# Performance work log

Hardware: AMD Instinct MI355X
Metric: run time of the kernel (lower is better)

The kernel has to match this reference:

```python
import jax, jax.numpy as jnp
import numpy as np

N_NODES = 100000
N_EDGES = 3200000
IN_DIM = 64
HID = 64


def setup_inputs() -> dict:
    key = jax.random.key(0)
    ks = jax.random.split(key, 12)
    x = jax.random.normal(ks[0], (N_NODES, IN_DIM), dtype=jnp.float32)
    edge_index = jax.random.randint(ks[1], (2, N_EDGES), 0, N_NODES, dtype=jnp.int64)
    tau = jax.random.uniform(ks[2], (N_NODES, 1), dtype=jnp.float32)
    d1 = IN_DIM + 1  # augmented feature dim
    s1 = 1.0 / np.sqrt(d1)
    s2 = 1.0 / np.sqrt(HID)
    # SAGEConv: out = lin_l(mean_aggr) + lin_r(x); bias lives in lin_l. Weights stored [in, out].
    W1l = jax.random.uniform(ks[3], (d1, HID), jnp.float32, -s1, s1)
    b1l = jax.random.uniform(ks[4], (HID,), jnp.float32, -s1, s1)
    W1r = jax.random.uniform(ks[5], (d1, HID), jnp.float32, -s1, s1)
    W2l = jax.random.uniform(ks[6], (HID, HID), jnp.float32, -s2, s2)
    b2l = jax.random.uniform(ks[7], (HID,), jnp.float32, -s2, s2)
    W2r = jax.random.uniform(ks[8], (HID, HID), jnp.float32, -s2, s2)
    Wfc = jax.random.uniform(ks[9], (HID, 1), jnp.float32, -s2, s2)
    bfc = jax.random.uniform(ks[10], (1,), jnp.float32, -s2, s2)
    return {"x": x, "edge_index": edge_index, "tau": tau,
            "W1l": W1l, "b1l": b1l, "W1r": W1r,
            "W2l": W2l, "b2l": b2l, "W2r": W2r,
            "Wfc": Wfc, "bfc": bfc}


def _sage_conv(x, src, dst, Wl, bl, Wr, n_nodes):
    # mean aggregation of source-node features onto target nodes
    summed = jax.ops.segment_sum(x[src], dst, num_segments=n_nodes)  # [N, d]
    deg = jax.ops.segment_sum(jnp.ones(src.shape[0], x.dtype), dst, num_segments=n_nodes)
    mean = summed / jnp.maximum(deg, 1.0)[:, None]
    return mean @ Wl + bl + x @ Wr


def reference(x, edge_index, tau, W1l, b1l, W1r, W2l, b2l, W2r, Wfc, bfc):
    src, dst = edge_index[0], edge_index[1]
    n = x.shape[0]
    h = jnp.concatenate([x, tau], axis=1)  # augment_features: append tau column
    h = jax.nn.relu(_sage_conv(h, src, dst, W1l, b1l, W1r, n))
    h = jax.nn.relu(_sage_conv(h, src, dst, W2l, b2l, W2r, n))
    return h @ Wfc + bfc  # [N, 1]
```

## Files before the change

### kernel.cpp

```cpp
#include <hip/hip_runtime.h>
#include <hip/hip_bf16.h>
#include <hip/hip_fp16.h>
#include <hip/hip_fp8.h>


#define BSH 7
#define NBKT 782
#define NBLK 512
#define PER 6250
#define CAP 6144
#define AB2 256

typedef _Float16 half8 __attribute__((ext_vector_type(8)));
typedef float floatx4 __attribute__((ext_vector_type(4)));
typedef float floatx2 __attribute__((ext_vector_type(2)));

struct h4s { __half2 lo, hi; };

#if __has_builtin(__builtin_amdgcn_cvt_pk_f32_fp8)
template <bool HI>
__device__ __forceinline__ float2 f8x2_to_f2(int v) {
    floatx2 r = __builtin_amdgcn_cvt_pk_f32_fp8(v, HI);
    return make_float2(r.x, r.y);
}
#else
template <bool HI>
__device__ __forceinline__ float2 f8x2_to_f2(int v) {
    unsigned short u = HI ? (unsigned short)(((unsigned)v) >> 16)
                          : (unsigned short)(v & 0xFFFF);
    __half2_raw r = __hip_cvt_fp8x2_to_halfraw2((__hip_fp8x2_storage_t)u, __HIP_E4M3);
    return __half22float2(*(__half2*)&r);
}
#endif

#if __has_builtin(__builtin_amdgcn_cvt_pk_fp8_f32)
__device__ __forceinline__ unsigned f4_to_f8x4(float a, float b, float c, float d) {
    int lo = __builtin_amdgcn_cvt_pk_fp8_f32(a, b, 0, false);
    return (unsigned)__builtin_amdgcn_cvt_pk_fp8_f32(c, d, lo, true);
}
__device__ __forceinline__ unsigned char f_to_f8(float a) {
    return (unsigned char)(__builtin_amdgcn_cvt_pk_fp8_f32(a, a, 0, false) & 0xFF);
}
#else
__device__ __forceinline__ unsigned f4_to_f8x4(float a, float b, float c, float d) {
    unsigned lo = (unsigned)__hip_cvt_float2_to_fp8x2(make_float2(a, b), __HIP_SATFINITE, __HIP_E4M3);
    unsigned hi = (unsigned)__hip_cvt_float2_to_fp8x2(make_float2(c, d), __HIP_SATFINITE, __HIP_E4M3);
    return lo | (hi << 16);
}
__device__ __forceinline__ unsigned char f_to_f8(float a) {
    return (unsigned char)__hip_cvt_float_to_fp8(a, __HIP_SATFINITE, __HIP_E4M3);
}
#endif

__global__ __launch_bounds__(256) void k_histprep(
    const int* __restrict__ dst, int* __restrict__ histT, int E,
    const float* __restrict__ x, __half* __restrict__ xh,
    unsigned char* __restrict__ xf8, int n4,
    const float* __restrict__ W1l, const float* __restrict__ W1r,
    const float* __restrict__ W2l, const float* __restrict__ W2r,
    __half* __restrict__ wbuf1, __half* __restrict__ wbuf2) {
    if (blockIdx.x < NBLK) {
        __shared__ int h[NBKT];
        for (int i = threadIdx.x; i < NBKT; i += 256) h[i] = 0;
        __syncthreads();
        int lo = blockIdx.x * PER;
        int hi = lo + PER; if (hi > E) hi = E;
        for (int e = lo + threadIdx.x; e < hi; e += 256)
            atomicAdd(&h[dst[e] >> BSH], 1);
        __syncthreads();
        for (int k = threadIdx.x; k < NBKT; k += 256)
            histT[k * NBLK + blockIdx.x] = h[k];
    } else if (blockIdx.x < NBLK + 9) {
        int idx = (blockIdx.x - NBLK) * 256 + threadIdx.x;
        if (idx < 1280) {
            int lane = idx & 63;
            int nt = (idx >> 6) & 3;
            int kstep = idx >> 8;
            int col = nt * 16 + (lane & 15);
            int kbase = kstep * 32 + (lane >> 4) * 8;
#pragma unroll
            for (int j = 0; j < 8; ++j) {
                int k = kbase + j;
                float v;
                if (k < 64)        v = W1l[k * 64 + col];
                else if (k < 128)  v = W1r[(k - 64) * 64 + col];
                else if (k == 128) v = W1l[64 * 64 + col];
                else if (k == 129) v = W1r[64 * 64 + col];
                else v = 0.f;
                wbuf1[(size_t)idx * 8 + j] = __float2half(v);
            }
        } else if (idx < 1280 + 1024) {
            int i2 = idx - 1280;
            int lane = i2 & 63;
            int nt = (i2 >> 6) & 3;
            int kstep = i2 >> 8;
            int col = nt * 16 + (lane & 15);
            int kbase = kstep * 32 + (lane >> 4) * 8;
#pragma unroll
            for (int j = 0; j < 8; ++j) {
                int k = kbase + j;
                float v = (k < 64) ? W2l[k * 64 + col] : W2r[(k - 64) * 64 + col];
                wbuf2[(size_t)i2 * 8 + j] = __float2half(v);
            }
        }
    } else {
        int i = (blockIdx.x - NBLK - 9) * 256 + threadIdx.x;
        if (i < n4) {
            float4 v = ((const float4*)x)[i];
            ((__half2*)xh)[2 * i]     = __floats2half2_rn(v.x, v.y);
            ((__half2*)xh)[2 * i + 1] = __floats2half2_rn(v.z, v.w);
            ((unsigned*)xf8)[i] = f4_to_f8x4(v.x, v.y, v.z, v.w);
        }
    }
}


__global__ __launch_bounds__(NBLK) void k_scanblk(int* __restrict__ histT,
                                                  int* __restrict__ btot) {
    __shared__ int s[NBLK];
    int k = blockIdx.x, t = threadIdx.x;
    int v = histT[k * NBLK + t];
    s[t] = v;
    __syncthreads();
    for (int off = 1; off < NBLK; off <<= 1) {
        int u = (t >= off) ? s[t - off] : 0;
        __syncthreads();
        s[t] += u;
        __syncthreads();
    }
    histT[k * NBLK + t] = s[t] - v;
    if (t == NBLK - 1) btot[k] = s[t];
}

__global__ __launch_bounds__(1024) void k_scanbkt(const int* __restrict__ btot,
                                                  int* __restrict__ bstart) {
    __shared__ int s[1024];
    int t = threadIdx.x;
    int v = (t < NBKT) ? btot[t] : 0;
    s[t] = v;
    __syncthreads();
    for (int off = 1; off < 1024; off <<= 1) {
        int u = (t >= off) ? s[t - off] : 0;
        __syncthreads();
        s[t] += u;
        __syncthreads();
    }
    if (t < NBKT) bstart[t] = s[t] - v;
    if (t == NBKT - 1) bstart[NBKT] = s[t];
}

__global__ __launch_bounds__(256) void k_scatter(const int* __restrict__ src,
                                                 const int* __restrict__ dst,
                                                 const int* __restrict__ histT,
                                                 const int* __restrict__ bstart,
                                                 int* __restrict__ binned, int E) {
    __shared__ int sorted[PER];
    __shared__ int lstart[NBKT + 1];
    __shared__ int cur[NBKT];
    __shared__ int gst[NBKT];
    __shared__ int tsum[256];
    int b = blockIdx.x, t = threadIdx.x;
    int base = b * PER;
    int blen = E - base; if (blen > PER) blen = PER;

    for (int k = t; k < NBKT; k += 256) lstart[k] = 0;
    __syncthreads();
    for (int e = base + t; e < base + blen; e += 256)
        atomicAdd(&lstart[dst[e] >> BSH], 1);
    __syncthreads();
    int c0 = 0;
    int i0 = t * 4;
#pragma unroll
    for (int j = 0; j < 4; ++j)
        if (i0 + j < NBKT) c0 += lstart[i0 + j];
    tsum[t] = c0;
    __syncthreads();
    for (int off = 1; off < 256; off <<= 1) {
        int u = (t >= off) ? tsum[t - off] : 0;
        __syncthreads();
        tsum[t] += u;
        __syncthreads();
    }
    int running = tsum[t] - c0;
    __syncthreads();
#pragma unroll
    for (int j = 0; j < 4; ++j) {
        int i = i0 + j;
        if (i < NBKT) {
            int v = lstart[i];
            lstart[i] = running;
            running += v;
        }
    }
    __syncthreads();
    if (t == 0) lstart[NBKT] = blen;
    for (int k = t; k < NBKT; k += 256) {
        cur[k] = lstart[k];
        gst[k] = bstart[k] + histT[k * NBLK + b];
    }
    __syncthreads();
    for (int e = base + t; e < base + blen; e += 256) {
        int d = dst[e], s = src[e];
        int pos = atomicAdd(&cur[d >> BSH], 1);
        sorted[pos] = (s << BSH) | (d & ((1 << BSH) - 1));
    }
    __syncthreads();
    int qw = t >> 4, ql = t & 15;
    for (int k = qw; k < NBKT; k += 16) {
        int st = lstart[k];
        int ln = lstart[k + 1] - st;
        int gd = gst[k];
        for (int i = ql; i < ln; i += 16)
            binned[gd + i] = sorted[st + i];
    }
}

__global__ __launch_bounds__(512) void k_csr(int* __restrict__ binned,
                                             const int* __restrict__ bstart,
                                             int* __restrict__ nodeoff,
                                             int E, int N) {
    __shared__ int cnt[128], sarr[128], cur[128];
    __shared__ int sorted[CAP];
    int k = blockIdx.x, t = threadIdx.x;
    int lo = bstart[k], hi = bstart[k + 1];
    if (t < 128) cnt[t] = 0;
    __syncthreads();
    for (int eb = lo; eb < hi; eb += 512 * 4) {
        int e0 = eb + t, e1 = e0 + 512, e2 = e0 + 1024, e3 = e0 + 1536;
        int p0 = (e0 < hi) ? binned[e0] : -1;
        int p1 = (e1 < hi) ? binned[e1] : -1;
        int p2 = (e2 < hi) ? binned[e2] : -1;
        int p3 = (e3 < hi) ? binned[e3] : -1;
        if (p0 >= 0) atomicAdd(&cnt[p0 & 127], 1);
        if (p1 >= 0) atomicAdd(&cnt[p1 & 127], 1);
        if (p2 >= 0) atomicAdd(&cnt[p2 & 127], 1);
        if (p3 >= 0) atomicAdd(&cnt[p3 & 127], 1);
    }
    __syncthreads();
    if (t < 128) sarr[t] = cnt[t];
    __syncthreads();
    for (int off = 1; off < 128; off <<= 1) {
        int u = 0;
        if (t < 128 && t >= off) u = sarr[t - off];
        __syncthreads();
        if (t < 128) sarr[t] += u;
        __syncthreads();
    }
    if (t < 128) {
        int excl = sarr[t] - cnt[t];
        cur[t] = excl;
        int node = (k << BSH) + t;
        if (node < N) nodeoff[node] = lo + excl;
    }
    if (k == NBKT - 1 && t == 0) nodeoff[N] = E;
    __syncthreads();
    for (int eb = lo; eb < hi; eb += 512 * 4) {
        int e0 = eb + t, e1 = e0 + 512, e2 = e0 + 1024, e3 = e0 + 1536;
        int p0 = (e0 < hi) ? binned[e0] : -1;
        int p1 = (e1 < hi) ? binned[e1] : -1;
        int p2 = (e2 < hi) ? binned[e2] : -1;
        int p3 = (e3 < hi) ? binned[e3] : -1;
        if (p0 >= 0) { int pos = atomicAdd(&cur[p0 & 127], 1); if (pos < CAP) sorted[pos] = p0 >> BSH; }
        if (p1 >= 0) { int pos = atomicAdd(&cur[p1 & 127], 1); if (pos < CAP) sorted[pos] = p1 >> BSH; }
        if (p2 >= 0) { int pos = atomicAdd(&cur[p2 & 127], 1); if (pos < CAP) sorted[pos] = p2 >> BSH; }
        if (p3 >= 0) { int pos = atomicAdd(&cur[p3 & 127], 1); if (pos < CAP) sorted[pos] = p3 >> BSH; }
    }
    __syncthreads();
    int len = hi - lo; if (len > CAP) len = CAP;
    for (int i = t; i < len; i += 512)
        binned[lo + i] = sorted[i];
}


__global__ __launch_bounds__(AB2) void k_aggrb1(
    const int* __restrict__ nbr, const int* __restrict__ nodeoff,
    const unsigned char* __restrict__ xf8, const float* __restrict__ tau,
    __half* __restrict__ zm1, __half* __restrict__ mt1, int N) {
    int t = threadIdx.x;
    int lane = t & 63;
    int q = lane >> 4;
    int c = lane & 15;
    int g = c & 3;
    int ch = c >> 2;
    unsigned cb = (unsigned)(ch << 4);
    const char* xb = (const char*)xf8;
    int nb = blockIdx.x << 6;

    for (int p = (t >> 6); p < 16; p += (AB2 / 64)) {
        int ld = (p << 2) + q;
        int node = nb + ld;
        int off0 = 0, off1 = 0;
        if (node < N) { off0 = nodeoff[node]; off1 = nodeoff[node + 1]; }
        int d = off1 - off0;
        int dm = d;
        dm = max(dm, __shfl_xor(dm, 16, 64));
        dm = max(dm, __shfl_xor(dm, 32, 64));
        float4 A0 = {0.f, 0.f, 0.f, 0.f}, A1 = A0, A2 = A0, A3 = A0;
        float sumtau = 0.f;
        for (int base = 0; base < dm; base += 16) {
            int nmax = dm - base; if (nmax > 16) nmax = 16;
            int ng = (nmax + 3) >> 2;
            int s0 = base + g;
            int s1 = s0 + 4, s2 = s0 + 8, s3 = s0 + 12;
            bool v0 = s0 < d, v1 = s1 < d, v2 = s2 < d, v3 = s3 < d;
            int sx0, sx1, sx2, sx3;
            int4 r0, r1, r2, r3;
            sx0 = nbr[off0 + (v0 ? s0 : 0)];
            sx0 = v0 ? sx0 : 0;
            r0 = *(const int4*)(xb + (((unsigned)sx0 << 6) + cb));
            if (ng > 1) {
                sx1 = nbr[off0 + (v1 ? s1 : 0)];
                sx1 = v1 ? sx1 : 0;
                r1 = *(const int4*)(xb + (((unsigned)sx1 << 6) + cb));
            }
            if (ng > 2) {
                sx2 = nbr[off0 + (v2 ? s2 : 0)];
                sx2 = v2 ? sx2 : 0;
                r2 = *(const int4*)(xb + (((unsigned)sx2 << 6) + cb));
            }
            if (ng > 3) {
                sx3 = nbr[off0 + (v3 ? s3 : 0)];
                sx3 = v3 ? sx3 : 0;
                r3 = *(const int4*)(xb + (((unsigned)sx3 << 6) + cb));
            }
            if (ch == 0) {
                if (v0) sumtau += tau[sx0];
                if (ng > 1 && v1) sumtau += tau[sx1];
                if (ng > 2 && v2) sumtau += tau[sx2];
                if (ng > 3 && v3) sumtau += tau[sx3];
            }
            auto accum = [&](const int4& r) {
                float2 l0 = f8x2_to_f2<false>(r.x), h0 = f8x2_to_f2<true>(r.x);
                float2 l1 = f8x2_to_f2<false>(r.y), h1v = f8x2_to_f2<true>(r.y);
                float2 l2 = f8x2_to_f2<false>(r.z), h2v = f8x2_to_f2<true>(r.z);
                float2 l3 = f8x2_to_f2<false>(r.w), h3v = f8x2_to_f2<true>(r.w);
                A0.x += l0.x; A0.y += l0.y; A0.z += h0.x; A0.w += h0.y;
                A1.x += l1.x; A1.y += l1.y; A1.z += h1v.x; A1.w += h1v.y;
                A2.x += l2.x; A2.y += l2.y; A2.z += h2v.x; A2.w += h2v.y;
                A3.x += l3.x; A3.y += l3.y; A3.z += h3v.x; A3.w += h3v.y;
            };
            if (v0)            accum(r0);
            if (ng > 1 && v1)  accum(r1);
            if (ng > 2 && v2)  accum(r2);
            if (ng > 3 && v3)  accum(r3);
        }
#pragma unroll
        for (int off = 1; off <= 2; off <<= 1) {
            A0.x += __shfl_xor(A0.x, off, 64); A0.y += __shfl_xor(A0.y, off, 64);
            A0.z += __shfl_xor(A0.z, off, 64); A0.w += __shfl_xor(A0.w, off, 64);
            A1.x += __shfl_xor(A1.x, off, 64); A1.y += __shfl_xor(A1.y, off, 64);
            A1.z += __shfl_xor(A1.z, off, 64); A1.w += __shfl_xor(A1.w, off, 64);
            A2.x += __shfl_xor(A2.x, off, 64); A2.y += __shfl_xor(A2.y, off, 64);
            A2.z += __shfl_xor(A2.z, off, 64); A2.w += __shfl_xor(A2.w, off, 64);
            A3.x += __shfl_xor(A3.x, off, 64); A3.y += __shfl_xor(A3.y, off, 64);
            A3.z += __shfl_xor(A3.z, off, 64); A3.w += __shfl_xor(A3.w, off, 64);
            sumtau += __shfl_xor(sumtau, off, 64);
        }
        float inv = 1.f / fmaxf((float)d, 1.f);
        if (node < N) {
            float4 Aw = (g == 0) ? A0 : ((g == 1) ? A1 : ((g == 2) ? A2 : A3));
            h4s o;
            o.lo = __floats2half2_rn(Aw.x * inv, Aw.y * inv);
            o.hi = __floats2half2_rn(Aw.z * inv, Aw.w * inv);
            *(h4s*)(zm1 + (size_t)node * 64 + (ch << 4) + (g << 2)) = o;
            if (c == 0) mt1[node] = __float2half(sumtau * inv);
        }
    }
}

__global__ __launch_bounds__(AB2) void k_aggrb2(
    const int* __restrict__ nbr, const int* __restrict__ nodeoff,
    const unsigned char* __restrict__ h1f8, __half* __restrict__ zm2, int N) {
    int t = threadIdx.x;
    int lane = t & 63;
    int q = lane >> 4;
    int c = lane & 15;
    int g = c & 3;
    int ch = c >> 2;
    unsigned cb = (unsigned)(ch << 4);
    const char* hb = (const char*)h1f8;
    int nb = blockIdx.x << 6;

    for (int p = (t >> 6); p < 16; p += (AB2 / 64)) {
        int ld = (p << 2) + q;
        int node = nb + ld;
        int off0 = 0, off1 = 0;
        if (node < N) { off0 = nodeoff[node]; off1 = nodeoff[node + 1]; }
        int d = off1 - off0;
        int dm = d;
        dm = max(dm, __shfl_xor(dm, 16, 64));
        dm = max(dm, __shfl_xor(dm, 32, 64));
        float4 A0 = {0.f, 0.f, 0.f, 0.f}, A1 = A0, A2 = A0, A3 = A0;
        for (int base = 0; base < dm; base += 16) {
            int nmax = dm - base; if (nmax > 16) nmax = 16;
            int ng = (nmax + 3) >> 2;
            int s0 = base + g;
            int s1 = s0 + 4, s2 = s0 + 8, s3 = s0 + 12;
            bool v0 = s0 < d, v1 = s1 < d, v2 = s2 < d, v3 = s3 < d;
            int sx0, sx1, sx2, sx3;
            int4 r0, r1, r2, r3;
            sx0 = nbr[off0 + (v0 ? s0 : 0)];
            sx0 = v0 ? sx0 : 0;
            r0 = *(const int4*)(hb + (((unsigned)sx0 << 6) + cb));
            if (ng > 1) {
                sx1 = nbr[off0 + (v1 ? s1 : 0)];
                sx1 = v1 ? sx1 : 0;
                r1 = *(const int4*)(hb + (((unsigned)sx1 << 6) + cb));
            }
            if (ng > 2) {
                sx2 = nbr[off0 + (v2 ? s2 : 0)];
                sx2 = v2 ? sx2 : 0;
                r2 = *(const int4*)(hb + (((unsigned)sx2 << 6) + cb));
            }
            if (ng > 3) {
                sx3 = nbr[off0 + (v3 ? s3 : 0)];
                sx3 = v3 ? sx3 : 0;
                r3 = *(const int4*)(hb + (((unsigned)sx3 << 6) + cb));
            }
            auto accum = [&](const int4& r) {
                float2 l0 = f8x2_to_f2<false>(r.x), h0 = f8x2_to_f2<true>(r.x);
                float2 l1 = f8x2_to_f2<false>(r.y), h1v = f8x2_to_f2<true>(r.y);
                float2 l2 = f8x2_to_f2<false>(r.z), h2v = f8x2_to_f2<true>(r.z);
                float2 l3 = f8x2_to_f2<false>(r.w), h3v = f8x2_to_f2<true>(r.w);
                A0.x += l0.x; A0.y += l0.y; A0.z += h0.x; A0.w += h0.y;
                A1.x += l1.x; A1.y += l1.y; A1.z += h1v.x; A1.w += h1v.y;
                A2.x += l2.x; A2.y += l2.y; A2.z += h2v.x; A2.w += h2v.y;
                A3.x += l3.x; A3.y += l3.y; A3.z += h3v.x; A3.w += h3v.y;
            };
            if (v0)            accum(r0);
            if (ng > 1 && v1)  accum(r1);
            if (ng > 2 && v2)  accum(r2);
            if (ng > 3 && v3)  accum(r3);
        }
#pragma unroll
        for (int off = 1; off <= 2; off <<= 1) {
            A0.x += __shfl_xor(A0.x, off, 64); A0.y += __shfl_xor(A0.y, off, 64);
            A0.z += __shfl_xor(A0.z, off, 64); A0.w += __shfl_xor(A0.w, off, 64);
            A1.x += __shfl_xor(A1.x, off, 64); A1.y += __shfl_xor(A1.y, off, 64);
            A1.z += __shfl_xor(A1.z, off, 64); A1.w += __shfl_xor(A1.w, off, 64);
            A2.x += __shfl_xor(A2.x, off, 64); A2.y += __shfl_xor(A2.y, off, 64);
            A2.z += __shfl_xor(A2.z, off, 64); A2.w += __shfl_xor(A2.w, off, 64);
            A3.x += __shfl_xor(A3.x, off, 64); A3.y += __shfl_xor(A3.y, off, 64);
            A3.z += __shfl_xor(A3.z, off, 64); A3.w += __shfl_xor(A3.w, off, 64);
        }
        float inv = 1.f / fmaxf((float)d, 1.f);
        if (node < N) {
            float4 Aw = (g == 0) ? A0 : ((g == 1) ? A1 : ((g == 2) ? A2 : A3));
            h4s o;
            o.lo = __floats2half2_rn(Aw.x * inv, Aw.y * inv);
            o.hi = __floats2half2_rn(Aw.z * inv, Aw.w * inv);
            *(h4s*)(zm2 + (size_t)node * 64 + (ch << 4) + (g << 2)) = o;
        }
    }
}


__global__ __launch_bounds__(256) void k_gemm1(
    const __half* __restrict__ zm1, const __half* __restrict__ mt1,
    const __half* __restrict__ xh, const float* __restrict__ tau,
    const __half* __restrict__ wbuf1, const float* __restrict__ b1l,
    __half* __restrict__ h1, unsigned char* __restrict__ h1f8, int ntiles) {
    int tile = blockIdx.x * 4 + (threadIdx.x >> 6);
    if (tile >= ntiles) return;
    int lane = threadIdx.x & 63;
    int sub = lane & 15;
    int quad = lane >> 4;
    int row = tile * 16 + sub;

    floatx4 acc0 = {0.f, 0.f, 0.f, 0.f};
    floatx4 acc1 = {0.f, 0.f, 0.f, 0.f};
    floatx4 acc2 = {0.f, 0.f, 0.f, 0.f};
    floatx4 acc3 = {0.f, 0.f, 0.f, 0.f};

    const _Float16* zrow = (const _Float16*)zm1 + (size_t)row * 64 + quad * 8;
    const _Float16* xrow = (const _Float16*)xh + (size_t)row * 64 + quad * 8;
    const _Float16* wb = (const _Float16*)wbuf1 + (size_t)lane * 8;

    half8 amat[5];
    amat[0] = *(const half8*)(zrow);
    amat[1] = *(const half8*)(zrow + 32);
    amat[2] = *(const half8*)(xrow);
    amat[3] = *(const half8*)(xrow + 32);
    half8 a4 = {0, 0, 0, 0, 0, 0, 0, 0};
    if (quad == 0) {
        a4[0] = ((const _Float16*)mt1)[row];
        a4[1] = (_Float16)tau[row];
    }
    amat[4] = a4;

#pragma unroll
    for (int ks = 0; ks < 5; ++ks) {
        half8 a = amat[ks];
        half8 b0 = *(const half8*)(wb + (size_t)(ks * 4 + 0) * 512);
        half8 b1 = *(const half8*)(wb + (size_t)(ks * 4 + 1) * 512);
        half8 b2 = *(const half8*)(wb + (size_t)(ks * 4 + 2) * 512);
        half8 b3 = *(const half8*)(wb + (size_t)(ks * 4 + 3) * 512);
        acc0 = __builtin_amdgcn_mfma_f32_16x16x32_f16(a, b0, acc0, 0, 0, 0);
        acc1 = __builtin_amdgcn_mfma_f32_16x16x32_f16(a, b1, acc1, 0, 0, 0);
        acc2 = __builtin_amdgcn_mfma_f32_16x16x32_f16(a, b2, acc2, 0, 0, 0);
        acc3 = __builtin_amdgcn_mfma_f32_16x16x32_f16(a, b3, acc3, 0, 0, 0);
    }
    float bv0 = b1l[sub], bv1 = b1l[16 + sub], bv2 = b1l[32 + sub], bv3 = b1l[48 + sub];
#pragma unroll
    for (int reg = 0; reg < 4; ++reg) {
        int r = quad * 4 + reg;
        float v0 = fmaxf(acc0[reg] + bv0, 0.f);
        float v1 = fmaxf(acc1[reg] + bv1, 0.f);
        float v2 = fmaxf(acc2[reg] + bv2, 0.f);
        float v3 = fmaxf(acc3[reg] + bv3, 0.f);
        __half* orow = h1 + (size_t)(tile * 16 + r) * 64;
        orow[sub]      = __float2half(v0);
        orow[16 + sub] = __float2half(v1);
        orow[32 + sub] = __float2half(v2);
        orow[48 + sub] = __float2half(v3);
        unsigned char* orow8 = h1f8 + (size_t)(tile * 16 + r) * 64;
        orow8[sub]      = f_to_f8(v0);
        orow8[16 + sub] = f_to_f8(v1);
        orow8[32 + sub] = f_to_f8(v2);
        orow8[48 + sub] = f_to_f8(v3);
    }
}

__global__ __launch_bounds__(256) void k_gemm2(
    const __half* __restrict__ zm2, const __half* __restrict__ h1,
    const __half* __restrict__ wbuf2, const float* __restrict__ b2l,
    const float* __restrict__ Wfc, const float* __restrict__ bfc,
    float* __restrict__ out, int ntiles) {
    int tile = blockIdx.x * 4 + (threadIdx.x >> 6);
    if (tile >= ntiles) return;
    int lane = threadIdx.x & 63;
    int sub = lane & 15;
    int quad = lane >> 4;
    int row = tile * 16 + sub;

    floatx4 acc0 = {0.f, 0.f, 0.f, 0.f};
    floatx4 acc1 = {0.f, 0.f, 0.f, 0.f};
    floatx4 acc2 = {0.f, 0.f, 0.f, 0.f};
    floatx4 acc3 = {0.f, 0.f, 0.f, 0.f};

    const _Float16* zrow = (const _Float16*)zm2 + (size_t)row * 64 + quad * 8;
    const _Float16* hrow = (const _Float16*)h1 + (size_t)row * 64 + quad * 8;
    const _Float16* wb = (const _Float16*)wbuf2 + (size_t)lane * 8;

    half8 amat[4];
    amat[0] = *(const half8*)(zrow);
    amat[1] = *(const half8*)(zrow + 32);
    amat[2] = *(const half8*)(hrow);
    amat[3] = *(const half8*)(hrow + 32);

#pragma unroll
    for (int ks = 0; ks < 4; ++ks) {
        half8 a = amat[ks];
        half8 b0 = *(const half8*)(wb + (size_t)(ks * 4 + 0) * 512);
        half8 b1 = *(const half8*)(wb + (size_t)(ks * 4 + 1) * 512);
        half8 b2 = *(const half8*)(wb + (size_t)(ks * 4 + 2) * 512);
        half8 b3 = *(const half8*)(wb + (size_t)(ks * 4 + 3) * 512);
        acc0 = __builtin_amdgcn_mfma_f32_16x16x32_f16(a, b0, acc0, 0, 0, 0);
        acc1 = __builtin_amdgcn_mfma_f32_16x16x32_f16(a, b1, acc1, 0, 0, 0);
        acc2 = __builtin_amdgcn_mfma_f32_16x16x32_f16(a, b2, acc2, 0, 0, 0);
        acc3 = __builtin_amdgcn_mfma_f32_16x16x32_f16(a, b3, acc3, 0, 0, 0);
    }
    float bb0 = b2l[sub], bb1 = b2l[16 + sub], bb2 = b2l[32 + sub], bb3 = b2l[48 + sub];
    float wv0 = Wfc[sub], wv1 = Wfc[16 + sub], wv2 = Wfc[32 + sub], wv3 = Wfc[48 + sub];
    float p[4];
#pragma unroll
    for (int reg = 0; reg < 4; ++reg) {
        p[reg] = fmaxf(acc0[reg] + bb0, 0.f) * wv0
               + fmaxf(acc1[reg] + bb1, 0.f) * wv1
               + fmaxf(acc2[reg] + bb2, 0.f) * wv2
               + fmaxf(acc3[reg] + bb3, 0.f) * wv3;
    }
#pragma unroll
    for (int m = 1; m <= 8; m <<= 1) {
#pragma unroll
        for (int reg = 0; reg < 4; ++reg) p[reg] += __shfl_xor(p[reg], m, 64);
    }
    if (sub == 0) {
        float b0 = bfc[0];
#pragma unroll
        for (int reg = 0; reg < 4; ++reg)
            out[tile * 16 + quad * 4 + reg] = p[reg] + b0;
    }
}

extern "C" void kernel_launch(void* const* d_in, const int* in_sizes, int n_in,
                              void* d_out, int out_size, void* d_ws, size_t ws_size,
                              hipStream_t stream) {
    const float* x   = (const float*)d_in[0];
    const int*   ei  = (const int*)d_in[1];
    const float* tau = (const float*)d_in[2];
    const float* W1l = (const float*)d_in[3];
    const float* b1l = (const float*)d_in[4];
    const float* W1r = (const float*)d_in[5];
    const float* W2l = (const float*)d_in[6];
    const float* b2l = (const float*)d_in[7];
    const float* W2r = (const float*)d_in[8];
    const float* Wfc = (const float*)d_in[9];
    const float* bfc = (const float*)d_in[10];
    float* out = (float*)d_out;

    const int N = in_sizes[0] / 64;
    const int E = in_sizes[1] / 2;
    const int* src = ei;
    const int* dst = ei + E;

    char* w = (char*)d_ws;
    auto take = [&](size_t b) { char* p = w; w += (b + 255) & ~(size_t)255; return p; };
    int*           histT  = (int*)take((size_t)NBKT * NBLK * 4);
    int*           btot   = (int*)take((size_t)NBKT * 4);
    int*           bstart = (int*)take((size_t)(NBKT + 1) * 4);
    int*           binned = (int*)take((size_t)(E + 64) * 4);
    int*           nodeoff= (int*)take((size_t)(N + 2) * 4);
    __half*        xh     = (__half*)take((size_t)N * 64 * 2);
    unsigned char* xf8    = (unsigned char*)take((size_t)N * 64);
    __half*        h1     = (__half*)take((size_t)N * 64 * 2);
    unsigned char* h1f8   = (unsigned char*)take((size_t)N * 64);
    __half*        zm1    = (__half*)take((size_t)N * 64 * 2);
    __half*        mt1    = (__half*)take((size_t)N * 2);
    __half*        zm2    = (__half*)take((size_t)N * 64 * 2);
    __half*        wbuf1  = (__half*)take(1280 * 8 * 2);
    __half*        wbuf2  = (__half*)take(1024 * 8 * 2);

    int n4 = N * 16;
    int hpblocks = NBLK + 9 + (n4 + 255) / 256;
    int ntiles = N / 16;
    int gblocks = (ntiles + 3) / 4;
    int ablocks = (N + 63) / 64;

    k_histprep<<<hpblocks, 256, 0, stream>>>(dst, histT, E, x, xh, xf8, n4,
                                             W1l, W1r, W2l, W2r, wbuf1, wbuf2);
    k_scanblk <<<NBKT, NBLK, 0, stream>>>(histT, btot);
    k_scanbkt <<<1, 1024, 0, stream>>>(btot, bstart);
    k_scatter <<<NBLK, 256, 0, stream>>>(src, dst, histT, bstart, binned, E);
    k_csr     <<<NBKT, 512, 0, stream>>>(binned, bstart, nodeoff, E, N);
    k_aggrb1  <<<ablocks, AB2, 0, stream>>>(binned, nodeoff, xf8, tau, zm1, mt1, N);
    k_gemm1   <<<gblocks, 256, 0, stream>>>(zm1, mt1, xh, tau, wbuf1, b1l, h1, h1f8, ntiles);
    k_aggrb2  <<<ablocks, AB2, 0, stream>>>(binned, nodeoff, h1f8, zm2, N);
    k_gemm2   <<<gblocks, 256, 0, stream>>>(zm2, h1, wbuf2, b2l, Wfc, bfc, out, ntiles);
}
```

Measured before the change: 273.9 us.

## Split fp8 feature tables into column halves so gathers fit in L2

The fp8 node feature tables (xf8, h1f8) are stored as two separate 32-byte-per-node halves. Each neighbor aggregation now runs as two launches of one templated kernel, one per column half, so each random-gather working set is half as large and more likely to stay cache-resident. The gather loop also prefetches the next neighbor indices and uses branch-free masking across 8 slots per node instead of 4. In exchange, the CSR neighbor list is read twice per layer and two extra kernel launches are added.

```diff
diff --git a/kernel.cpp b/kernel.cpp
--- a/kernel.cpp
+++ b/kernel.cpp
@@ -14,6 +14,7 @@
 typedef _Float16 half8 __attribute__((ext_vector_type(8)));
 typedef float floatx4 __attribute__((ext_vector_type(4)));
 typedef float floatx2 __attribute__((ext_vector_type(2)));
+typedef int intx4 __attribute__((ext_vector_type(4)));
 
 struct h4s { __half2 lo, hi; };
 
@@ -55,7 +56,7 @@
 __global__ __launch_bounds__(256) void k_histprep(
     const int* __restrict__ dst, int* __restrict__ histT, int E,
     const float* __restrict__ x, __half* __restrict__ xh,
-    unsigned char* __restrict__ xf8, int n4,
+    unsigned char* __restrict__ xf8a, unsigned char* __restrict__ xf8b, int n4,
     const float* __restrict__ W1l, const float* __restrict__ W1r,
     const float* __restrict__ W2l, const float* __restrict__ W2r,
     __half* __restrict__ wbuf1, __half* __restrict__ wbuf2) {
@@ -109,7 +110,11 @@
             float4 v = ((const float4*)x)[i];
             ((__half2*)xh)[2 * i]     = __floats2half2_rn(v.x, v.y);
             ((__half2*)xh)[2 * i + 1] = __floats2half2_rn(v.z, v.w);
-            ((unsigned*)xf8)[i] = f4_to_f8x4(v.x, v.y, v.z, v.w);
+            unsigned v8 = f4_to_f8x4(v.x, v.y, v.z, v.w);
+            int node = i >> 4;
+            int cq = i & 15;
+            if (cq < 8) ((unsigned*)xf8a)[node * 8 + cq] = v8;
+            else        ((unsigned*)xf8b)[node * 8 + (cq - 8)] = v8;
         }
     }
 }
@@ -271,19 +276,19 @@
         binned[lo + i] = sorted[i];
 }
 
-
-__global__ __launch_bounds__(AB2) void k_aggrb1(
+template <bool TAU>
+__global__ __launch_bounds__(AB2, 6) void k_aggrh(
     const int* __restrict__ nbr, const int* __restrict__ nodeoff,
-    const unsigned char* __restrict__ xf8, const float* __restrict__ tau,
-    __half* __restrict__ zm1, __half* __restrict__ mt1, int N) {
+    const unsigned char* __restrict__ feat, const float* __restrict__ tau,
+    __half* __restrict__ zm, int colbase, __half* __restrict__ mt1, int N) {
     int t = threadIdx.x;
     int lane = t & 63;
     int q = lane >> 4;
     int c = lane & 15;
-    int g = c & 3;
-    int ch = c >> 2;
-    unsigned cb = (unsigned)(ch << 4);
-    const char* xb = (const char*)xf8;
+    int g = c & 7;
+    int ch2 = c >> 3;
+    unsigned cb = (unsigned)(ch2 << 4);
+    const char* fb = (const char*)feat;
     int nb = blockIdx.x << 6;
 
     for (int p = (t >> 6); p < 16; p += (AB2 / 64)) {
@@ -297,55 +302,50 @@
         dm = max(dm, __shfl_xor(dm, 32, 64));
         float4 A0 = {0.f, 0.f, 0.f, 0.f}, A1 = A0, A2 = A0, A3 = A0;
         float sumtau = 0.f;
+        int base0 = off0 + g;
+        int nx0 = nbr[base0];
+        int nx1 = nbr[base0 + 8];
         for (int base = 0; base < dm; base += 16) {
-            int nmax = dm - base; if (nmax > 16) nmax = 16;
-            int ng = (nmax + 3) >> 2;
             int s0 = base + g;
-            int s1 = s0 + 4, s2 = s0 + 8, s3 = s0 + 12;
-            bool v0 = s0 < d, v1 = s1 < d, v2 = s2 < d, v3 = s3 < d;
-            int sx0, sx1, sx2, sx3;
-            int4 r0, r1, r2, r3;
-            sx0 = nbr[off0 + (v0 ? s0 : 0)];
-            sx0 = v0 ? sx0 : 0;
-            r0 = *(const int4*)(xb + (((unsigned)sx0 << 6) + cb));
-            if (ng > 1) {
-                sx1 = nbr[off0 + (v1 ? s1 : 0)];
-                sx1 = v1 ? sx1 : 0;
-                r1 = *(const int4*)(xb + (((unsigned)sx1 << 6) + cb));
+            bool v0 = s0 < d, v1 = s0 + 8 < d;
+            int cu0 = nx0, cu1 = nx1;
+            int bn = base0 + base + 16;
+            nx0 = nbr[bn];
+            nx1 = nbr[bn + 8];
+            int sx0 = v0 ? cu0 : 0;
+            int sx1 = v1 ? cu1 : 0;
+            intx4 r0 = *(const intx4*)(fb + (((unsigned)sx0 << 5) + cb));
+            intx4 r1 = *(const intx4*)(fb + (((unsigned)sx1 << 5) + cb));
+            if (TAU) {
+                float ta0 = tau[sx0], ta1 = tau[sx1];
+                sumtau += (v0 ? ta0 : 0.f) + (v1 ? ta1 : 0.f);
             }
-            if (ng > 2) {
-                sx2 = nbr[off0 + (v2 ? s2 : 0)];
-                sx2 = v2 ? sx2 : 0;
-                r2 = *(const int4*)(xb + (((unsigned)sx2 << 6) + cb));
-            }
-            if (ng > 3) {
-                sx3 = nbr[off0 + (v3 ? s3 : 0)];
-                sx3 = v3 ? sx3 : 0;
-                r3 = *(const int4*)(xb + (((unsigned)sx3 << 6) + cb));
-            }
-            if (ch == 0) {
-                if (v0) sumtau += tau[sx0];
-                if (ng > 1 && v1) sumtau += tau[sx1];
-                if (ng > 2 && v2) sumtau += tau[sx2];
-                if (ng > 3 && v3) sumtau += tau[sx3];
-            }
-            auto accum = [&](const int4& r) {
-                float2 l0 = f8x2_to_f2<false>(r.x), h0 = f8x2_to_f2<true>(r.x);
-                float2 l1 = f8x2_to_f2<false>(r.y), h1v = f8x2_to_f2<true>(r.y);
-                float2 l2 = f8x2_to_f2<false>(r.z), h2v = f8x2_to_f2<true>(r.z);
-                float2 l3 = f8x2_to_f2<false>(r.w), h3v = f8x2_to_f2<true>(r.w);
+            int m0 = v0 ? -1 : 0, m1 = v1 ? -1 : 0;
+            r0 &= (intx4){m0, m0, m0, m0};
+            r1 &= (intx4){m1, m1, m1, m1};
+            {
+                float2 l0 = f8x2_to_f2<false>(r0.x), h0 = f8x2_to_f2<true>(r0.x);
+                float2 l1 = f8x2_to_f2<false>(r0.y), h1v = f8x2_to_f2<true>(r0.y);
+                float2 l2 = f8x2_to_f2<false>(r0.z), h2v = f8x2_to_f2<true>(r0.z);
+                float2 l3 = f8x2_to_f2<false>(r0.w), h3v = f8x2_to_f2<true>(r0.w);
                 A0.x += l0.x; A0.y += l0.y; A0.z += h0.x; A0.w += h0.y;
                 A1.x += l1.x; A1.y += l1.y; A1.z += h1v.x; A1.w += h1v.y;
                 A2.x += l2.x; A2.y += l2.y; A2.z += h2v.x; A2.w += h2v.y;
                 A3.x += l3.x; A3.y += l3.y; A3.z += h3v.x; A3.w += h3v.y;
-            };
-            if (v0)            accum(r0);
-            if (ng > 1 && v1)  accum(r1);
-            if (ng > 2 && v2)  accum(r2);
-            if (ng > 3 && v3)  accum(r3);
+            }
+            {
+                float2 l0 = f8x2_to_f2<false>(r1.x), h0 = f8x2_to_f2<true>(r1.x);
+                float2 l1 = f8x2_to_f2<false>(r1.y), h1v = f8x2_to_f2<true>(r1.y);
+                float2 l2 = f8x2_to_f2<false>(r1.z), h2v = f8x2_to_f2<true>(r1.z);
+                float2 l3 = f8x2_to_f2<false>(r1.w), h3v = f8x2_to_f2<true>(r1.w);
+                A0.x += l0.x; A0.y += l0.y; A0.z += h0.x; A0.w += h0.y;
+                A1.x += l1.x; A1.y += l1.y; A1.z += h1v.x; A1.w += h1v.y;
+                A2.x += l2.x; A2.y += l2.y; A2.z += h2v.x; A2.w += h2v.y;
+                A3.x += l3.x; A3.y += l3.y; A3.z += h3v.x; A3.w += h3v.y;
+            }
         }
 #pragma unroll
-        for (int off = 1; off <= 2; off <<= 1) {
+        for (int off = 1; off <= 4; off <<= 1) {
             A0.x += __shfl_xor(A0.x, off, 64); A0.y += __shfl_xor(A0.y, off, 64);
             A0.z += __shfl_xor(A0.z, off, 64); A0.w += __shfl_xor(A0.w, off, 64);
             A1.x += __shfl_xor(A1.x, off, 64); A1.y += __shfl_xor(A1.y, off, 64);
@@ -354,103 +354,17 @@
             A2.z += __shfl_xor(A2.z, off, 64); A2.w += __shfl_xor(A2.w, off, 64);
             A3.x += __shfl_xor(A3.x, off, 64); A3.y += __shfl_xor(A3.y, off, 64);
             A3.z += __shfl_xor(A3.z, off, 64); A3.w += __shfl_xor(A3.w, off, 64);
-            sumtau += __shfl_xor(sumtau, off, 64);
+            if (TAU) sumtau += __shfl_xor(sumtau, off, 64);
         }
         float inv = 1.f / fmaxf((float)d, 1.f);
-        if (node < N) {
+        if (node < N && g < 4) {
             float4 Aw = (g == 0) ? A0 : ((g == 1) ? A1 : ((g == 2) ? A2 : A3));
             h4s o;
             o.lo = __floats2half2_rn(Aw.x * inv, Aw.y * inv);
             o.hi = __floats2half2_rn(Aw.z * inv, Aw.w * inv);
-            *(h4s*)(zm1 + (size_t)node * 64 + (ch << 4) + (g << 2)) = o;
-            if (c == 0) mt1[node] = __float2half(sumtau * inv);
+            *(h4s*)(zm + (size_t)node * 64 + colbase + (ch2 << 4) + (g << 2)) = o;
         }
-    }
-}
-
-__global__ __launch_bounds__(AB2) void k_aggrb2(
-    const int* __restrict__ nbr, const int* __restrict__ nodeoff,
-    const unsigned char* __restrict__ h1f8, __half* __restrict__ zm2, int N) {
-    int t = threadIdx.x;
-    int lane = t & 63;
-    int q = lane >> 4;
-    int c = lane & 15;
-    int g = c & 3;
-    int ch = c >> 2;
-    unsigned cb = (unsigned)(ch << 4);
-    const char* hb = (const char*)h1f8;
-    int nb = blockIdx.x << 6;
-
-    for (int p = (t >> 6); p < 16; p += (AB2 / 64)) {
-        int ld = (p << 2) + q;
-        int node = nb + ld;
-        int off0 = 0, off1 = 0;
-        if (node < N) { off0 = nodeoff[node]; off1 = nodeoff[node + 1]; }
-        int d = off1 - off0;
-        int dm = d;
-        dm = max(dm, __shfl_xor(dm, 16, 64));
-        dm = max(dm, __shfl_xor(dm, 32, 64));
-        float4 A0 = {0.f, 0.f, 0.f, 0.f}, A1 = A0, A2 = A0, A3 = A0;
-        for (int base = 0; base < dm; base += 16) {
-            int nmax = dm - base; if (nmax > 16) nmax = 16;
-            int ng = (nmax + 3) >> 2;
-            int s0 = base + g;
-            int s1 = s0 + 4, s2 = s0 + 8, s3 = s0 + 12;
-            bool v0 = s0 < d, v1 = s1 < d, v2 = s2 < d, v3 = s3 < d;
-            int sx0, sx1, sx2, sx3;
-            int4 r0, r1, r2, r3;
-            sx0 = nbr[off0 + (v0 ? s0 : 0)];
-            sx0 = v0 ? sx0 : 0;
-            r0 = *(const int4*)(hb + (((unsigned)sx0 << 6) + cb));
-            if (ng > 1) {
-                sx1 = nbr[off0 + (v1 ? s1 : 0)];
-                sx1 = v1 ? sx1 : 0;
-                r1 = *(const int4*)(hb + (((unsigned)sx1 << 6) + cb));
-            }
-            if (ng > 2) {
-                sx2 = nbr[off0 + (v2 ? s2 : 0)];
-                sx2 = v2 ? sx2 : 0;
-                r2 = *(const int4*)(hb + (((unsigned)sx2 << 6) + cb));
-            }
-            if (ng > 3) {
-                sx3 = nbr[off0 + (v3 ? s3 : 0)];
-                sx3 = v3 ? sx3 : 0;
-                r3 = *(const int4*)(hb + (((unsigned)sx3 << 6) + cb));
-            }
-            auto accum = [&](const int4& r) {
-                float2 l0 = f8x2_to_f2<false>(r.x), h0 = f8x2_to_f2<true>(r.x);
-                float2 l1 = f8x2_to_f2<false>(r.y), h1v = f8x2_to_f2<true>(r.y);
-                float2 l2 = f8x2_to_f2<false>(r.z), h2v = f8x2_to_f2<true>(r.z);
-                float2 l3 = f8x2_to_f2<false>(r.w), h3v = f8x2_to_f2<true>(r.w);
-                A0.x += l0.x; A0.y += l0.y; A0.z += h0.x; A0.w += h0.y;
-                A1.x += l1.x; A1.y += l1.y; A1.z += h1v.x; A1.w += h1v.y;
-                A2.x += l2.x; A2.y += l2.y; A2.z += h2v.x; A2.w += h2v.y;
-                A3.x += l3.x; A3.y += l3.y; A3.z += h3v.x; A3.w += h3v.y;
-            };
-            if (v0)            accum(r0);
-            if (ng > 1 && v1)  accum(r1);
-            if (ng > 2 && v2)  accum(r2);
-            if (ng > 3 && v3)  accum(r3);
-        }
-#pragma unroll
-        for (int off = 1; off <= 2; off <<= 1) {
-            A0.x += __shfl_xor(A0.x, off, 64); A0.y += __shfl_xor(A0.y, off, 64);
-            A0.z += __shfl_xor(A0.z, off, 64); A0.w += __shfl_xor(A0.w, off, 64);
-            A1.x += __shfl_xor(A1.x, off, 64); A1.y += __shfl_xor(A1.y, off, 64);
-            A1.z += __shfl_xor(A1.z, off, 64); A1.w += __shfl_xor(A1.w, off, 64);
-            A2.x += __shfl_xor(A2.x, off, 64); A2.y += __shfl_xor(A2.y, off, 64);
-            A2.z += __shfl_xor(A2.z, off, 64); A2.w += __shfl_xor(A2.w, off, 64);
-            A3.x += __shfl_xor(A3.x, off, 64); A3.y += __shfl_xor(A3.y, off, 64);
-            A3.z += __shfl_xor(A3.z, off, 64); A3.w += __shfl_xor(A3.w, off, 64);
-        }
-        float inv = 1.f / fmaxf((float)d, 1.f);
-        if (node < N) {
-            float4 Aw = (g == 0) ? A0 : ((g == 1) ? A1 : ((g == 2) ? A2 : A3));
-            h4s o;
-            o.lo = __floats2half2_rn(Aw.x * inv, Aw.y * inv);
-            o.hi = __floats2half2_rn(Aw.z * inv, Aw.w * inv);
-            *(h4s*)(zm2 + (size_t)node * 64 + (ch << 4) + (g << 2)) = o;
-        }
+        if (TAU && node < N && c == 0) mt1[node] = __float2half(sumtau * inv);
     }
 }
 
@@ -459,7 +373,8 @@
     const __half* __restrict__ zm1, const __half* __restrict__ mt1,
     const __half* __restrict__ xh, const float* __restrict__ tau,
     const __half* __restrict__ wbuf1, const float* __restrict__ b1l,
-    __half* __restrict__ h1, unsigned char* __restrict__ h1f8, int ntiles) {
+    __half* __restrict__ h1, unsigned char* __restrict__ h1f8a,
+    unsigned char* __restrict__ h1f8b, int ntiles) {
     int tile = blockIdx.x * 4 + (threadIdx.x >> 6);
     if (tile >= ntiles) return;
     int lane = threadIdx.x & 63;
@@ -513,11 +428,12 @@
         orow[16 + sub] = __float2half(v1);
         orow[32 + sub] = __float2half(v2);
         orow[48 + sub] = __float2half(v3);
-        unsigned char* orow8 = h1f8 + (size_t)(tile * 16 + r) * 64;
-        orow8[sub]      = f_to_f8(v0);
-        orow8[16 + sub] = f_to_f8(v1);
-        orow8[32 + sub] = f_to_f8(v2);
-        orow8[48 + sub] = f_to_f8(v3);
+        unsigned char* oa = h1f8a + (size_t)(tile * 16 + r) * 32;
+        unsigned char* ob = h1f8b + (size_t)(tile * 16 + r) * 32;
+        oa[sub]      = f_to_f8(v0);
+        oa[16 + sub] = f_to_f8(v1);
+        ob[sub]      = f_to_f8(v2);
+        ob[16 + sub] = f_to_f8(v3);
     }
 }
 
@@ -612,9 +528,11 @@
     int*           binned = (int*)take((size_t)(E + 64) * 4);
     int*           nodeoff= (int*)take((size_t)(N + 2) * 4);
     __half*        xh     = (__half*)take((size_t)N * 64 * 2);
-    unsigned char* xf8    = (unsigned char*)take((size_t)N * 64);
+    unsigned char* xf8a   = (unsigned char*)take((size_t)N * 32);
+    unsigned char* xf8b   = (unsigned char*)take((size_t)N * 32);
     __half*        h1     = (__half*)take((size_t)N * 64 * 2);
-    unsigned char* h1f8   = (unsigned char*)take((size_t)N * 64);
+    unsigned char* h1f8a  = (unsigned char*)take((size_t)N * 32);
+    unsigned char* h1f8b  = (unsigned char*)take((size_t)N * 32);
     __half*        zm1    = (__half*)take((size_t)N * 64 * 2);
     __half*        mt1    = (__half*)take((size_t)N * 2);
     __half*        zm2    = (__half*)take((size_t)N * 64 * 2);
@@ -627,14 +545,16 @@
     int gblocks = (ntiles + 3) / 4;
     int ablocks = (N + 63) / 64;
 
-    k_histprep<<<hpblocks, 256, 0, stream>>>(dst, histT, E, x, xh, xf8, n4,
+    k_histprep<<<hpblocks, 256, 0, stream>>>(dst, histT, E, x, xh, xf8a, xf8b, n4,
                                              W1l, W1r, W2l, W2r, wbuf1, wbuf2);
     k_scanblk <<<NBKT, NBLK, 0, stream>>>(histT, btot);
     k_scanbkt <<<1, 1024, 0, stream>>>(btot, bstart);
     k_scatter <<<NBLK, 256, 0, stream>>>(src, dst, histT, bstart, binned, E);
     k_csr     <<<NBKT, 512, 0, stream>>>(binned, bstart, nodeoff, E, N);
-    k_aggrb1  <<<ablocks, AB2, 0, stream>>>(binned, nodeoff, xf8, tau, zm1, mt1, N);
-    k_gemm1   <<<gblocks, 256, 0, stream>>>(zm1, mt1, xh, tau, wbuf1, b1l, h1, h1f8, ntiles);
-    k_aggrb2  <<<ablocks, AB2, 0, stream>>>(binned, nodeoff, h1f8, zm2, N);
+    k_aggrh<true>  <<<ablocks, AB2, 0, stream>>>(binned, nodeoff, xf8a, tau, zm1, 0, mt1, N);
+    k_aggrh<false> <<<ablocks, AB2, 0, stream>>>(binned, nodeoff, xf8b, tau, zm1, 32, mt1, N);
+    k_gemm1   <<<gblocks, 256, 0, stream>>>(zm1, mt1, xh, tau, wbuf1, b1l, h1, h1f8a, h1f8b, ntiles);
+    k_aggrh<false> <<<ablocks, AB2, 0, stream>>>(binned, nodeoff, h1f8a, tau, zm2, 0, mt1, N);
+    k_aggrh<false> <<<ablocks, AB2, 0, stream>>>(binned, nodeoff, h1f8b, tau, zm2, 32, mt1, N);
     k_gemm2   <<<gblocks, 256, 0, stream>>>(zm2, h1, wbuf2, b2l, Wfc, bfc, out, ntiles);
 }
```

New measurement: 306.9 us. 12.0% more time.
